# Optimization experiments

Measured on AMD Instinct MI355X. Metric: run time of the kernel, lower is better.

Reference implementation:

```python
import jax, jax.numpy as jnp
import numpy as np

GENE_NUM = 3000
N_NODES = 50000
N_EDGES = 1000000
DIM = 128


def setup_inputs() -> dict:
    key = jax.random.key(0)
    ks = jax.random.split(key, 8)
    h = jax.random.normal(ks[0], (N_NODES, DIM), dtype=jnp.float32)
    alpha = jax.random.normal(ks[1], (GENE_NUM + 2,), dtype=jnp.float32)
    edge_weight = jax.random.uniform(ks[2], (N_EDGES,), dtype=jnp.float32)
    # Xavier-uniform Linear weight, zero bias
    gain = float(np.sqrt(2.0))  # calculate_gain('relu')
    bound = gain * np.sqrt(6.0 / (DIM + DIM))
    W = jax.random.uniform(ks[3], (DIM, DIM), minval=-bound, maxval=bound, dtype=jnp.float32)
    b = jnp.zeros((DIM,), dtype=jnp.float32)
    # node ids: genes 0..GENE_NUM-1 have id = gene index (>=0); cells have id = -1 (<0)
    node_id = jnp.concatenate([
        jnp.arange(GENE_NUM, dtype=jnp.int64),
        -jnp.ones((N_NODES - GENE_NUM,), dtype=jnp.int64),
    ])
    edge_src = jax.random.randint(ks[4], (N_EDGES,), 0, N_NODES, dtype=jnp.int64)
    edge_dst = jax.random.randint(ks[5], (N_EDGES,), 0, N_NODES, dtype=jnp.int64)
    return {"h": h, "alpha": alpha, "edge_weight": edge_weight, "W": W, "b": b,
            "node_id": node_id, "edge_src": edge_src, "edge_dst": edge_dst}


def reference(h, alpha, edge_weight, W, b, node_id, edge_src, edge_dst):
    gene_num = alpha.shape[0] - 2
    src_id = node_id[edge_src]  # [E]
    dst_id = node_id[edge_dst]  # [E]
    # default: cell self-loop alpha -> index gene_num + 1
    idx = jnp.full(edge_src.shape, gene_num + 1, dtype=jnp.int32)
    idx = jnp.where((src_id >= 0) & (dst_id < 0), src_id.astype(jnp.int32), idx)   # gene->cell: beta[src]
    idx = jnp.where((dst_id >= 0) & (src_id < 0), dst_id.astype(jnp.int32), idx)   # cell->gene: beta[dst]
    idx = jnp.where((dst_id >= 0) & (src_id >= 0), gene_num, idx)                  # gene self-loop alpha
    # gather -> per-edge message [E, D]
    coeff = alpha[idx] * edge_weight                     # [E]
    msg = h[edge_src] * coeff[:, None]                   # [E, D]
    # scatter-mean over destination nodes
    n = h.shape[0]
    summ = jax.ops.segment_sum(msg, edge_dst, num_segments=n)           # [N, D]
    cnt = jax.ops.segment_sum(jnp.ones_like(edge_weight), edge_dst, num_segments=n)
    neigh = summ / jnp.maximum(cnt, 1.0)[:, None]
    # MLP: dropout(eval, identity) -> Linear -> ReLU -> norm(identity)
    z = jax.nn.relu(neigh @ W.T + b)
    return z
```

## Files before the change

kernel.cpp:

```cpp
#include <hip/hip_runtime.h>

#define D 128
#define PSHIFT 6
#define PSIZE 64
#define EDGES_PER_BLK 4096
#define CAP 2048
#define MAXPART 1024
#define NCHUNK 4

typedef __attribute__((ext_vector_type(8))) short bf16x8;
typedef __attribute__((ext_vector_type(4))) float f32x4;

__device__ __forceinline__ unsigned short f2bf(float f) {
  unsigned int u = __float_as_uint(f);
  u = (u + 0x7fffu + ((u >> 16) & 1)) >> 16;
  return (unsigned short)u;
}

__global__ __launch_bounds__(512) void cvt_hist_kernel(
    const float* __restrict__ h, unsigned short* __restrict__ h16, int total4,
    const int* __restrict__ edst, int* __restrict__ g_hist, int E,
    int cvtBlocks, int N) {
  if ((int)blockIdx.x < cvtBlocks) {
    int i = blockIdx.x * 512 + threadIdx.x;
    if (i >= total4) return;
    float4 v = ((const float4*)h)[i];
    ushort4 o;
    o.x = f2bf(v.x); o.y = f2bf(v.y); o.z = f2bf(v.z); o.w = f2bf(v.w);
    int f = i * 4;
    int n = f >> 7;
    int d = f & 127;
    int c = d >> 5;
    int wi = d & 31;
    ((ushort4*)h16)[(size_t)c * N * 8 + n * 8 + (wi >> 2)] = o;
    return;
  }
  __shared__ int cnt[MAXPART];
  int t = threadIdx.x;
  cnt[t] = 0; cnt[t + 512] = 0;
  __syncthreads();
  int eb = (blockIdx.x - cvtBlocks) * EDGES_PER_BLK;
#pragma unroll
  for (int q = 0; q < 8; ++q) {
    int e = eb + q * 512 + t;
    if (e < E) atomicAdd(&cnt[edst[e] >> PSHIFT], 1);
  }
  __syncthreads();
  int c = cnt[t];
  if (c > 0) atomicAdd(&g_hist[t], c);
  c = cnt[t + 512];
  if (c > 0) atomicAdd(&g_hist[t + 512], c);
}

__global__ __launch_bounds__(512) void part_scan_kernel(
    const int* __restrict__ g_hist, int* __restrict__ part_off,
    int* __restrict__ g_cursor, int E, int npart) {
  __shared__ int ts[512];
  int t = threadIdx.x;
  int i0 = 2 * t, i1 = 2 * t + 1;
  int v0 = (i0 < npart) ? g_hist[i0] : 0;
  int v1 = (i1 < npart) ? g_hist[i1] : 0;
  ts[t] = v0 + v1;
  __syncthreads();
  for (int off = 1; off < 512; off <<= 1) {
    int x = (t >= off) ? ts[t - off] : 0;
    __syncthreads();
    ts[t] += x;
    __syncthreads();
  }
  int excl = ts[t] - (v0 + v1);
  if (i0 < npart) { part_off[i0] = excl; g_cursor[i0] = excl; }
  if (i1 < npart) { part_off[i1] = excl + v0; g_cursor[i1] = excl + v0; }
  if (t == 0) part_off[npart] = E;
}

__global__ __launch_bounds__(512) void bin_scatter_kernel(
    const float* __restrict__ alpha, const float* __restrict__ ew,
    const int* __restrict__ node_id, const int* __restrict__ esrc,
    const int* __restrict__ edst, int* __restrict__ g_cursor,
    int2* __restrict__ recs, int E, int gene_num) {
  __shared__ int2 lrec[EDGES_PER_BLK];
  __shared__ unsigned short lbin[EDGES_PER_BLK];
  __shared__ int cnt[MAXPART], offl[MAXPART], gbase[MAXPART];
  __shared__ int ts[512];

  int t = threadIdx.x;
  cnt[t] = 0; cnt[t + 512] = 0;
  __syncthreads();

  int eb = blockIdx.x * EDGES_PER_BLK;
  int rx[8]; float rc[8]; int rb[8]; int rk[8];
#pragma unroll
  for (int q = 0; q < 8; ++q) {
    int e = eb + q * 512 + t;
    rk[q] = -1;
    if (e < E) {
      int src = esrc[e];
      int dst = edst[e];
      int sid = node_id[src];
      int did = node_id[dst];
      int idx;
      if (sid >= 0) idx = (did >= 0) ? gene_num : sid;
      else          idx = (did >= 0) ? did : (gene_num + 1);
      rc[q] = alpha[idx] * ew[e];
      rx[q] = src | ((dst & (PSIZE - 1)) << 16);
      int b = dst >> PSHIFT;
      rb[q] = b;
      rk[q] = atomicAdd(&cnt[b], 1);
    }
  }
  __syncthreads();

  int c0 = cnt[2 * t], c1 = cnt[2 * t + 1];
  ts[t] = c0 + c1;
  __syncthreads();
  for (int off = 1; off < 512; off <<= 1) {
    int x = (t >= off) ? ts[t - off] : 0;
    __syncthreads();
    ts[t] += x;
    __syncthreads();
  }
  int exclp = ts[t] - (c0 + c1);
  offl[2 * t] = exclp;
  offl[2 * t + 1] = exclp + c0;
  __syncthreads();

#pragma unroll
  for (int q = 0; q < 8; ++q) {
    if (rk[q] >= 0) {
      int ls = offl[rb[q]] + rk[q];
      lrec[ls] = make_int2(rx[q], __float_as_int(rc[q]));
      lbin[ls] = (unsigned short)rb[q];
    }
  }
  __syncthreads();

  {
    int c = cnt[t];
    if (c > 0) gbase[t] = atomicAdd(&g_cursor[t], c);
    c = cnt[t + 512];
    if (c > 0) gbase[t + 512] = atomicAdd(&g_cursor[t + 512], c);
  }
  __syncthreads();

  int tot = E - eb;
  if (tot > EDGES_PER_BLK) tot = EDGES_PER_BLK;
  for (int s = t; s < tot; s += 512) {
    int b = lbin[s];
    recs[gbase[b] + (s - offl[b])] = lrec[s];
  }
}

__global__ __launch_bounds__(512) void part_acc_kernel(
    const unsigned short* __restrict__ h16, const int2* __restrict__ recs,
    const int* __restrict__ part_off, float* __restrict__ neigh, int N) {
  __shared__ int2 lrec[CAP];
  __shared__ int cnt[PSIZE], offl[PSIZE];

  int t = threadIdx.x;
  int p = blockIdx.x >> 2;
  int chunk = blockIdx.x & 3;
  if (t < PSIZE) cnt[t] = 0;
  __syncthreads();

  int start = part_off[p];
  int R = part_off[p + 1] - start;
  if (R > CAP) R = CAP;

  int2 rq[4]; int dlq[4]; int rkq[4];
#pragma unroll
  for (int q = 0; q < 4; ++q) {
    int s = q * 512 + t;
    rkq[q] = -1;
    if (s < R) {
      int2 r = recs[start + s];
      rq[q] = r;
      int dl = (r.x >> 16) & (PSIZE - 1);
      dlq[q] = dl;
      rkq[q] = atomicAdd(&cnt[dl], 1);
    }
  }
  __syncthreads();

  if (t < PSIZE) offl[t] = cnt[t];
  __syncthreads();
  for (int off = 1; off < PSIZE; off <<= 1) {
    int x = 0;
    if (t < PSIZE && t >= off) x = offl[t - off];
    __syncthreads();
    if (t < PSIZE) offl[t] += x;
    __syncthreads();
  }
  if (t < PSIZE) offl[t] -= cnt[t];
  __syncthreads();

#pragma unroll
  for (int q = 0; q < 4; ++q)
    if (rkq[q] >= 0) lrec[offl[dlq[q]] + rkq[q]] = rq[q];
  __syncthreads();

  int w = t >> 6;
  int l = t & 63;
  int esub = l >> 4;
  int dpair = l & 15;
  const unsigned int* hp = ((const unsigned int*)h16) + (size_t)chunk * N * 16 + dpair;

  for (int dd = 0; dd < 4; ++dd) {
    int dlA = w * 8 + 2 * dd;
    int dlB = dlA + 1;
    int cA = cnt[dlA], oA = offl[dlA];
    int cB = cnt[dlB], oB = offl[dlB];
    float axA = 0.f, ayA = 0.f, axB = 0.f, ayB = 0.f;
    int cmax = (cA > cB) ? cA : cB;
    for (int k = 0; k < cmax; k += 16) {
      float cfA[4], cfB[4];
      unsigned int vA[4], vB[4];
      int aA[4], aB[4];
#pragma unroll
      for (int q = 0; q < 4; ++q) {
        int sl = k + 4 * q + esub;
        int iA = oA + sl; iA = (iA < CAP) ? iA : (CAP - 1);
        int iB = oB + sl; iB = (iB < CAP) ? iB : (CAP - 1);
        int2 rA = lrec[iA];
        int2 rB = lrec[iB];
        bool okA = sl < cA;
        bool okB = sl < cB;
        aA[q] = okA ? (rA.x & 0xffff) : 0;
        aB[q] = okB ? (rB.x & 0xffff) : 0;
        cfA[q] = okA ? __int_as_float(rA.y) : 0.f;
        cfB[q] = okB ? __int_as_float(rB.y) : 0.f;
      }
#pragma unroll
      for (int q = 0; q < 4; ++q) {
        vA[q] = hp[(size_t)aA[q] * 16];
        vB[q] = hp[(size_t)aB[q] * 16];
      }
#pragma unroll
      for (int q = 0; q < 4; ++q) {
        axA += cfA[q] * __uint_as_float(vA[q] << 16);
        ayA += cfA[q] * __uint_as_float(vA[q] & 0xffff0000u);
        axB += cfB[q] * __uint_as_float(vB[q] << 16);
        ayB += cfB[q] * __uint_as_float(vB[q] & 0xffff0000u);
      }
    }
    axA += __shfl_xor(axA, 16); ayA += __shfl_xor(ayA, 16);
    axB += __shfl_xor(axB, 16); ayB += __shfl_xor(ayB, 16);
    axA += __shfl_xor(axA, 32); ayA += __shfl_xor(ayA, 32);
    axB += __shfl_xor(axB, 32); ayB += __shfl_xor(ayB, 32);

    int dstA = p * PSIZE + dlA;
    int dstB = p * PSIZE + dlB;
    if (l < 16) {
      if (dstA < N) {
        float inv = 1.0f / (float)(cA > 0 ? cA : 1);
        ((float2*)neigh)[(size_t)dstA * 64 + chunk * 16 + dpair] =
            make_float2(axA * inv, ayA * inv);
      }
      if (dstB < N) {
        float inv = 1.0f / (float)(cB > 0 ? cB : 1);
        ((float2*)neigh)[(size_t)dstB * 64 + chunk * 16 + dpair] =
            make_float2(axB * inv, ayB * inv);
      }
    }
  }
}

__global__ __launch_bounds__(256) void mlp_mfma_kernel(
    const float* __restrict__ W, const float* __restrict__ bias,
    float* __restrict__ io, int N) {
  __shared__ __align__(16) unsigned short Wl[128 * 128];

  int t = threadIdx.x;
#pragma unroll
  for (int i = 0; i < 8; ++i) {
    int chunk = t + 256 * i;
    int row = chunk >> 4;
    int cb = chunk & 15;
    const float* gp = W + (size_t)row * 128 + cb * 8;
    float4 a = *(const float4*)gp;
    float4 b = *(const float4*)(gp + 4);
    bf16x8 v;
    v[0] = (short)f2bf(a.x); v[1] = (short)f2bf(a.y);
    v[2] = (short)f2bf(a.z); v[3] = (short)f2bf(a.w);
    v[4] = (short)f2bf(b.x); v[5] = (short)f2bf(b.y);
    v[6] = (short)f2bf(b.z); v[7] = (short)f2bf(b.w);
    *(bf16x8*)((char*)Wl + row * 256 + ((cb ^ (row & 7)) << 4)) = v;
  }
  __syncthreads();

  int l = t & 63;
  int w = t >> 6;
  int kg = l >> 4;
  int m_base = blockIdx.x * 64 + w * 16;
  int arow = m_base + (l & 15);
  if (arow >= N) arow = N - 1;

  bf16x8 af[4];
  const float* ap = io + (size_t)arow * 128 + kg * 8;
#pragma unroll
  for (int kk = 0; kk < 4; ++kk) {
    float4 a = *(const float4*)(ap + kk * 32);
    float4 b = *(const float4*)(ap + kk * 32 + 4);
    bf16x8 v;
    v[0] = (short)f2bf(a.x); v[1] = (short)f2bf(a.y);
    v[2] = (short)f2bf(a.z); v[3] = (short)f2bf(a.w);
    v[4] = (short)f2bf(b.x); v[5] = (short)f2bf(b.y);
    v[6] = (short)f2bf(b.z); v[7] = (short)f2bf(b.w);
    af[kk] = v;
  }

#pragma unroll
  for (int c = 0; c < 8; ++c) {
    f32x4 acc = {0.f, 0.f, 0.f, 0.f};
    int row_w = c * 16 + (l & 15);
    int rs = row_w & 7;
#pragma unroll
    for (int kk = 0; kk < 4; ++kk) {
      int cb = kk * 4 + kg;
      bf16x8 bf = *(bf16x8*)((char*)Wl + row_w * 256 + ((cb ^ rs) << 4));
      acc = __builtin_amdgcn_mfma_f32_16x16x32_bf16(af[kk], bf, acc, 0, 0, 0);
    }
    int j = c * 16 + (l & 15);
    float bj = bias[j];
#pragma unroll
    for (int r = 0; r < 4; ++r) {
      int m = m_base + kg * 4 + r;
      if (m < N) io[(size_t)m * 128 + j] = fmaxf(acc[r] + bj, 0.0f);
    }
  }
}

extern "C" void kernel_launch(void* const* d_in, const int* in_sizes, int n_in,
                              void* d_out, int out_size, void* d_ws, size_t ws_size,
                              hipStream_t stream) {
  const float* h     = (const float*)d_in[0];
  const float* alpha = (const float*)d_in[1];
  const float* ew    = (const float*)d_in[2];
  const float* W     = (const float*)d_in[3];
  const float* bias  = (const float*)d_in[4];
  const int* node_id = (const int*)d_in[5];
  const int* esrc    = (const int*)d_in[6];
  const int* edst    = (const int*)d_in[7];
  float* out = (float*)d_out;

  int E = in_sizes[2];
  int N = in_sizes[5];
  int gene_num = in_sizes[1] - 2;
  int npart = (N + PSIZE - 1) / PSIZE;
  int eblocks = (E + EDGES_PER_BLK - 1) / EDGES_PER_BLK;
  int total4 = N * D / 4;
  int cvtBlocks = (total4 + 511) / 512;

  int* g_hist   = (int*)d_ws;
  int* part_off = g_hist + MAXPART;
  int* g_cursor = part_off + MAXPART + 1;
  size_t h16_off = ((size_t)(3 * MAXPART + 1) * sizeof(int) + 15) & ~(size_t)15;
  unsigned short* h16 = (unsigned short*)((char*)d_ws + h16_off);
  size_t rec_off = (h16_off + (size_t)N * D * sizeof(unsigned short) + 15) & ~(size_t)15;
  int2* recs = (int2*)((char*)d_ws + rec_off);
  size_t need = rec_off + (size_t)E * sizeof(int2);
  if (ws_size < need) return;

  hipMemsetAsync(g_hist, 0, MAXPART * sizeof(int), stream);

  cvt_hist_kernel<<<cvtBlocks + eblocks, 512, 0, stream>>>(
      h, h16, total4, edst, g_hist, E, cvtBlocks, N);
  part_scan_kernel<<<1, 512, 0, stream>>>(g_hist, part_off, g_cursor, E, npart);
  bin_scatter_kernel<<<eblocks, 512, 0, stream>>>(alpha, ew, node_id, esrc,
                                                  edst, g_cursor, recs, E,
                                                  gene_num);
  part_acc_kernel<<<npart * NCHUNK, 512, 0, stream>>>(h16, recs, part_off, out, N);
  {
    int blocks = (N + 63) / 64;
    mlp_mfma_kernel<<<blocks, 256, 0, stream>>>(W, bias, out, N);
  }
}
```

Measured before the change: 117.8 us.

## Split per-partition local sort into its own kernel and pad segments to 16

The per-destination local sort that each of the four chunk blocks repeated is moved into a separate sort_kernel run once per partition. It writes the sorted records back and stores per-node counts and offsets to the workspace. The accumulation kernel now loads the pre-sorted records into zero-padded 16-aligned segments, which removes the per-element bounds clamps and lets each of the two destinations skip its loads once its own segment is done. This costs an extra kernel launch, an extra global read and write of the record array, and more shared memory per block.

```diff
diff --git a/kernel.cpp b/kernel.cpp
--- a/kernel.cpp
+++ b/kernel.cpp
@@ -5,6 +5,7 @@
 #define PSIZE 64
 #define EDGES_PER_BLK 4096
 #define CAP 2048
+#define CAPP 3072
 #define MAXPART 1024
 #define NCHUNK 4
 
@@ -151,15 +152,14 @@
   }
 }
 
-__global__ __launch_bounds__(512) void part_acc_kernel(
-    const unsigned short* __restrict__ h16, const int2* __restrict__ recs,
-    const int* __restrict__ part_off, float* __restrict__ neigh, int N) {
+__global__ __launch_bounds__(512) void sort_kernel(
+    int2* __restrict__ recs, const int* __restrict__ part_off,
+    int* __restrict__ cnt_g, int* __restrict__ off_g) {
   __shared__ int2 lrec[CAP];
   __shared__ int cnt[PSIZE], offl[PSIZE];
 
   int t = threadIdx.x;
-  int p = blockIdx.x >> 2;
-  int chunk = blockIdx.x & 3;
+  int p = blockIdx.x;
   if (t < PSIZE) cnt[t] = 0;
   __syncthreads();
 
@@ -199,48 +199,109 @@
     if (rkq[q] >= 0) lrec[offl[dlq[q]] + rkq[q]] = rq[q];
   __syncthreads();
 
+  for (int s = t; s < R; s += 512) recs[start + s] = lrec[s];
+  if (t < PSIZE) {
+    cnt_g[p * PSIZE + t] = cnt[t];
+    off_g[p * PSIZE + t] = offl[t];
+  }
+}
+
+__global__ __launch_bounds__(512) void part_acc_kernel(
+    const unsigned short* __restrict__ h16, const int2* __restrict__ recs,
+    const int* __restrict__ part_off, const int* __restrict__ cnt_g,
+    const int* __restrict__ off_g, float* __restrict__ neigh, int N) {
+  __shared__ int2 lrec[CAPP];
+  __shared__ int cnt[PSIZE], offl[PSIZE], padoff[PSIZE];
+
+  int t = threadIdx.x;
+  int p = blockIdx.x >> 2;
+  int chunk = blockIdx.x & 3;
+
+  int start = part_off[p];
+  int R = part_off[p + 1] - start;
+  if (R > CAP) R = CAP;
+
+  if (t < PSIZE) {
+    cnt[t] = cnt_g[p * PSIZE + t];
+    offl[t] = off_g[p * PSIZE + t];
+    padoff[t] = (cnt[t] + 15) & ~15;
+  }
+  {
+    int2 z = make_int2(0, 0);
+#pragma unroll
+    for (int q = 0; q < CAPP / 512; ++q) lrec[q * 512 + t] = z;
+  }
+  __syncthreads();
+  for (int off = 1; off < PSIZE; off <<= 1) {
+    int x = 0;
+    if (t < PSIZE && t >= off) x = padoff[t - off];
+    __syncthreads();
+    if (t < PSIZE) padoff[t] += x;
+    __syncthreads();
+  }
+  if (t < PSIZE) padoff[t] -= (cnt[t] + 15) & ~15;
+  __syncthreads();
+
+  for (int s = t; s < R; s += 512) {
+    int2 r = recs[start + s];
+    int dl = (r.x >> 16) & (PSIZE - 1);
+    lrec[padoff[dl] + (s - offl[dl])] = r;
+  }
+  __syncthreads();
+
   int w = t >> 6;
   int l = t & 63;
   int esub = l >> 4;
   int dpair = l & 15;
-  const unsigned int* hp = ((const unsigned int*)h16) + (size_t)chunk * N * 16 + dpair;
+  const unsigned int* hp =
+      ((const unsigned int*)h16) + (size_t)chunk * N * 16 + dpair;
 
   for (int dd = 0; dd < 4; ++dd) {
     int dlA = w * 8 + 2 * dd;
     int dlB = dlA + 1;
-    int cA = cnt[dlA], oA = offl[dlA];
-    int cB = cnt[dlB], oB = offl[dlB];
+    int cA = cnt[dlA], cB = cnt[dlB];
+    int oA = padoff[dlA], oB = padoff[dlB];
+    int cpA = (cA + 15) & ~15, cpB = (cB + 15) & ~15;
     float axA = 0.f, ayA = 0.f, axB = 0.f, ayB = 0.f;
-    int cmax = (cA > cB) ? cA : cB;
-    for (int k = 0; k < cmax; k += 16) {
+    int cpm = (cpA > cpB) ? cpA : cpB;
+    for (int k = 0; k < cpm; k += 16) {
+      bool doA = k < cpA;
+      bool doB = k < cpB;
+      unsigned int aA[4], aB[4], vA[4], vB[4];
       float cfA[4], cfB[4];
-      unsigned int vA[4], vB[4];
-      int aA[4], aB[4];
-#pragma unroll
-      for (int q = 0; q < 4; ++q) {
-        int sl = k + 4 * q + esub;
-        int iA = oA + sl; iA = (iA < CAP) ? iA : (CAP - 1);
-        int iB = oB + sl; iB = (iB < CAP) ? iB : (CAP - 1);
-        int2 rA = lrec[iA];
-        int2 rB = lrec[iB];
-        bool okA = sl < cA;
-        bool okB = sl < cB;
-        aA[q] = okA ? (rA.x & 0xffff) : 0;
-        aB[q] = okB ? (rB.x & 0xffff) : 0;
-        cfA[q] = okA ? __int_as_float(rA.y) : 0.f;
-        cfB[q] = okB ? __int_as_float(rB.y) : 0.f;
-      }
-#pragma unroll
-      for (int q = 0; q < 4; ++q) {
-        vA[q] = hp[(size_t)aA[q] * 16];
-        vB[q] = hp[(size_t)aB[q] * 16];
-      }
-#pragma unroll
-      for (int q = 0; q < 4; ++q) {
-        axA += cfA[q] * __uint_as_float(vA[q] << 16);
-        ayA += cfA[q] * __uint_as_float(vA[q] & 0xffff0000u);
-        axB += cfB[q] * __uint_as_float(vB[q] << 16);
-        ayB += cfB[q] * __uint_as_float(vB[q] & 0xffff0000u);
+      if (doA) {
+#pragma unroll
+        for (int q = 0; q < 4; ++q) {
+          int2 r = lrec[oA + k + 4 * q + esub];
+          aA[q] = r.x & 0xffff;
+          cfA[q] = __int_as_float(r.y);
+        }
+#pragma unroll
+        for (int q = 0; q < 4; ++q) vA[q] = hp[(size_t)aA[q] * 16];
+      }
+      if (doB) {
+#pragma unroll
+        for (int q = 0; q < 4; ++q) {
+          int2 r = lrec[oB + k + 4 * q + esub];
+          aB[q] = r.x & 0xffff;
+          cfB[q] = __int_as_float(r.y);
+        }
+#pragma unroll
+        for (int q = 0; q < 4; ++q) vB[q] = hp[(size_t)aB[q] * 16];
+      }
+      if (doA) {
+#pragma unroll
+        for (int q = 0; q < 4; ++q) {
+          axA += cfA[q] * __uint_as_float(vA[q] << 16);
+          ayA += cfA[q] * __uint_as_float(vA[q] & 0xffff0000u);
+        }
+      }
+      if (doB) {
+#pragma unroll
+        for (int q = 0; q < 4; ++q) {
+          axB += cfB[q] * __uint_as_float(vB[q] << 16);
+          ayB += cfB[q] * __uint_as_float(vB[q] & 0xffff0000u);
+        }
       }
     }
     axA += __shfl_xor(axA, 16); ayA += __shfl_xor(ayA, 16);
@@ -354,7 +415,10 @@
   int* g_hist   = (int*)d_ws;
   int* part_off = g_hist + MAXPART;
   int* g_cursor = part_off + MAXPART + 1;
-  size_t h16_off = ((size_t)(3 * MAXPART + 1) * sizeof(int) + 15) & ~(size_t)15;
+  int* cnt_g    = g_cursor + MAXPART;
+  int* off_g    = cnt_g + MAXPART * PSIZE;
+  size_t h16_off = ((size_t)(3 * MAXPART + 1 + 2 * MAXPART * PSIZE) * sizeof(int)
+                    + 15) & ~(size_t)15;
   unsigned short* h16 = (unsigned short*)((char*)d_ws + h16_off);
   size_t rec_off = (h16_off + (size_t)N * D * sizeof(unsigned short) + 15) & ~(size_t)15;
   int2* recs = (int2*)((char*)d_ws + rec_off);
@@ -369,7 +433,9 @@
   bin_scatter_kernel<<<eblocks, 512, 0, stream>>>(alpha, ew, node_id, esrc,
                                                   edst, g_cursor, recs, E,
                                                   gene_num);
-  part_acc_kernel<<<npart * NCHUNK, 512, 0, stream>>>(h16, recs, part_off, out, N);
+  sort_kernel<<<npart, 512, 0, stream>>>(recs, part_off, cnt_g, off_g);
+  part_acc_kernel<<<npart * NCHUNK, 512, 0, stream>>>(h16, recs, part_off,
+                                                      cnt_g, off_g, out, N);
   {
     int blocks = (N + 63) / 64;
     mlp_mfma_kernel<<<blocks, 256, 0, stream>>>(W, bias, out, N);
```

Measured after the change: 116.7 us. About the same (-0.9%).

## Sort records once per partition in separate kernel and pad per-destination lists

Applied to the files above, without the earlier changes.

Moves the per-partition counting sort of edge records by destination out of the accumulation kernel into a new sort_kernel. It runs once per partition instead of once per feature chunk, and writes the sorted records plus count, offset and padded-offset tables back to global memory. The accumulation kernel then places records into a zero-initialised shared buffer with each destination's list padded to a multiple of four. One 16-lane group then walks one destination's list without per-element bounds checks. This removes the four-fold redundant sort and the masking overhead, at the cost of an extra launch, an extra global round trip for the records, and possible load imbalance between destinations of different degree.

```diff
diff --git a/kernel.cpp b/kernel.cpp
--- a/kernel.cpp
+++ b/kernel.cpp
@@ -5,6 +5,7 @@
 #define PSIZE 64
 #define EDGES_PER_BLK 4096
 #define CAP 2048
+#define CAPP 2244
 #define MAXPART 1024
 #define NCHUNK 4
 
@@ -151,15 +152,15 @@
   }
 }
 
-__global__ __launch_bounds__(512) void part_acc_kernel(
-    const unsigned short* __restrict__ h16, const int2* __restrict__ recs,
-    const int* __restrict__ part_off, float* __restrict__ neigh, int N) {
+__global__ __launch_bounds__(512) void sort_kernel(
+    int2* __restrict__ recs, const int* __restrict__ part_off,
+    int* __restrict__ cnt_g, int* __restrict__ off_g,
+    int* __restrict__ pad_g) {
   __shared__ int2 lrec[CAP];
-  __shared__ int cnt[PSIZE], offl[PSIZE];
-
-  int t = threadIdx.x;
-  int p = blockIdx.x >> 2;
-  int chunk = blockIdx.x & 3;
+  __shared__ int cnt[PSIZE], offl[PSIZE], padl[PSIZE];
+
+  int t = threadIdx.x;
+  int p = blockIdx.x;
   if (t < PSIZE) cnt[t] = 0;
   __syncthreads();
 
@@ -182,85 +183,107 @@
   }
   __syncthreads();
 
-  if (t < PSIZE) offl[t] = cnt[t];
+  if (t < PSIZE) { offl[t] = cnt[t]; padl[t] = (cnt[t] + 3) & ~3; }
   __syncthreads();
   for (int off = 1; off < PSIZE; off <<= 1) {
-    int x = 0;
-    if (t < PSIZE && t >= off) x = offl[t - off];
-    __syncthreads();
-    if (t < PSIZE) offl[t] += x;
-    __syncthreads();
-  }
-  if (t < PSIZE) offl[t] -= cnt[t];
+    int x = 0, y = 0;
+    if (t < PSIZE && t >= off) { x = offl[t - off]; y = padl[t - off]; }
+    __syncthreads();
+    if (t < PSIZE) { offl[t] += x; padl[t] += y; }
+    __syncthreads();
+  }
+  if (t < PSIZE) {
+    offl[t] -= cnt[t];
+    padl[t] -= (cnt[t] + 3) & ~3;
+  }
   __syncthreads();
 
 #pragma unroll
   for (int q = 0; q < 4; ++q)
     if (rkq[q] >= 0) lrec[offl[dlq[q]] + rkq[q]] = rq[q];
+  __syncthreads();
+
+  for (int s = t; s < R; s += 512) recs[start + s] = lrec[s];
+  if (t < PSIZE) {
+    cnt_g[p * PSIZE + t] = cnt[t];
+    off_g[p * PSIZE + t] = offl[t];
+    pad_g[p * PSIZE + t] = padl[t];
+  }
+}
+
+__global__ __launch_bounds__(512) void part_acc_kernel(
+    const unsigned short* __restrict__ h16, const int2* __restrict__ recs,
+    const int* __restrict__ part_off, const int* __restrict__ cnt_g,
+    const int* __restrict__ off_g, const int* __restrict__ pad_g,
+    float* __restrict__ neigh, int N) {
+  __shared__ int2 lrec[CAPP];
+  __shared__ int cnt[PSIZE], offl[PSIZE], padl[PSIZE];
+
+  int t = threadIdx.x;
+  int p = blockIdx.x >> 2;
+  int chunk = blockIdx.x & 3;
+
+  int start = part_off[p];
+  int R = part_off[p + 1] - start;
+  if (R > CAP) R = CAP;
+
+  if (t < PSIZE) {
+    cnt[t] = cnt_g[p * PSIZE + t];
+    offl[t] = off_g[p * PSIZE + t];
+    padl[t] = pad_g[p * PSIZE + t];
+  }
+  {
+    int2 z = make_int2(0, 0);
+    for (int q = t; q < CAPP; q += 512) lrec[q] = z;
+  }
+  __syncthreads();
+
+  for (int s = t; s < R; s += 512) {
+    int2 r = recs[start + s];
+    int dl = (r.x >> 16) & (PSIZE - 1);
+    lrec[padl[dl] + (s - offl[dl])] = r;
+  }
   __syncthreads();
 
   int w = t >> 6;
   int l = t & 63;
   int esub = l >> 4;
   int dpair = l & 15;
-  const unsigned int* hp = ((const unsigned int*)h16) + (size_t)chunk * N * 16 + dpair;
-
-  for (int dd = 0; dd < 4; ++dd) {
-    int dlA = w * 8 + 2 * dd;
-    int dlB = dlA + 1;
-    int cA = cnt[dlA], oA = offl[dlA];
-    int cB = cnt[dlB], oB = offl[dlB];
-    float axA = 0.f, ayA = 0.f, axB = 0.f, ayB = 0.f;
-    int cmax = (cA > cB) ? cA : cB;
-    for (int k = 0; k < cmax; k += 16) {
-      float cfA[4], cfB[4];
-      unsigned int vA[4], vB[4];
-      int aA[4], aB[4];
-#pragma unroll
-      for (int q = 0; q < 4; ++q) {
-        int sl = k + 4 * q + esub;
-        int iA = oA + sl; iA = (iA < CAP) ? iA : (CAP - 1);
-        int iB = oB + sl; iB = (iB < CAP) ? iB : (CAP - 1);
-        int2 rA = lrec[iA];
-        int2 rB = lrec[iB];
-        bool okA = sl < cA;
-        bool okB = sl < cB;
-        aA[q] = okA ? (rA.x & 0xffff) : 0;
-        aB[q] = okB ? (rB.x & 0xffff) : 0;
-        cfA[q] = okA ? __int_as_float(rA.y) : 0.f;
-        cfB[q] = okB ? __int_as_float(rB.y) : 0.f;
-      }
-#pragma unroll
-      for (int q = 0; q < 4; ++q) {
-        vA[q] = hp[(size_t)aA[q] * 16];
-        vB[q] = hp[(size_t)aB[q] * 16];
-      }
-#pragma unroll
-      for (int q = 0; q < 4; ++q) {
-        axA += cfA[q] * __uint_as_float(vA[q] << 16);
-        ayA += cfA[q] * __uint_as_float(vA[q] & 0xffff0000u);
-        axB += cfB[q] * __uint_as_float(vB[q] << 16);
-        ayB += cfB[q] * __uint_as_float(vB[q] & 0xffff0000u);
-      }
-    }
-    axA += __shfl_xor(axA, 16); ayA += __shfl_xor(ayA, 16);
-    axB += __shfl_xor(axB, 16); ayB += __shfl_xor(ayB, 16);
-    axA += __shfl_xor(axA, 32); ayA += __shfl_xor(ayA, 32);
-    axB += __shfl_xor(axB, 32); ayB += __shfl_xor(ayB, 32);
-
-    int dstA = p * PSIZE + dlA;
-    int dstB = p * PSIZE + dlB;
-    if (l < 16) {
-      if (dstA < N) {
-        float inv = 1.0f / (float)(cA > 0 ? cA : 1);
-        ((float2*)neigh)[(size_t)dstA * 64 + chunk * 16 + dpair] =
-            make_float2(axA * inv, ayA * inv);
-      }
-      if (dstB < N) {
-        float inv = 1.0f / (float)(cB > 0 ? cB : 1);
-        ((float2*)neigh)[(size_t)dstB * 64 + chunk * 16 + dpair] =
-            make_float2(axB * inv, ayB * inv);
-      }
+  const unsigned int* hpc =
+      ((const unsigned int*)h16) + (size_t)chunk * N * 16 + dpair;
+
+#pragma unroll
+  for (int h2 = 0; h2 < 2; ++h2) {
+    int myDl = w * 8 + h2 * 4 + esub;
+    int myCnt = cnt[myDl];
+    int myOff = padl[myDl];
+    int myPad = (myCnt + 3) & ~3;
+    float ax = 0.f, ay = 0.f;
+    for (int k = 0; k < myPad; k += 4) {
+      int2 r0 = lrec[myOff + k + 0];
+      int2 r1 = lrec[myOff + k + 1];
+      int2 r2 = lrec[myOff + k + 2];
+      int2 r3 = lrec[myOff + k + 3];
+      unsigned int v0 = hpc[(size_t)(r0.x & 0xffff) * 16];
+      unsigned int v1 = hpc[(size_t)(r1.x & 0xffff) * 16];
+      unsigned int v2 = hpc[(size_t)(r2.x & 0xffff) * 16];
+      unsigned int v3 = hpc[(size_t)(r3.x & 0xffff) * 16];
+      float c0 = __int_as_float(r0.y), c1 = __int_as_float(r1.y);
+      float c2 = __int_as_float(r2.y), c3 = __int_as_float(r3.y);
+      ax += c0 * __uint_as_float(v0 << 16);
+      ay += c0 * __uint_as_float(v0 & 0xffff0000u);
+      ax += c1 * __uint_as_float(v1 << 16);
+      ay += c1 * __uint_as_float(v1 & 0xffff0000u);
+      ax += c2 * __uint_as_float(v2 << 16);
+      ay += c2 * __uint_as_float(v2 & 0xffff0000u);
+      ax += c3 * __uint_as_float(v3 << 16);
+      ay += c3 * __uint_as_float(v3 & 0xffff0000u);
+    }
+    int dst = p * PSIZE + myDl;
+    if (dst < N) {
+      float inv = 1.0f / (float)(myCnt > 0 ? myCnt : 1);
+      ((float2*)neigh)[(size_t)dst * 64 + chunk * 16 + dpair] =
+          make_float2(ax * inv, ay * inv);
     }
   }
 }
@@ -354,7 +377,11 @@
   int* g_hist   = (int*)d_ws;
   int* part_off = g_hist + MAXPART;
   int* g_cursor = part_off + MAXPART + 1;
-  size_t h16_off = ((size_t)(3 * MAXPART + 1) * sizeof(int) + 15) & ~(size_t)15;
+  int* cnt_g    = g_cursor + MAXPART;
+  int* off_g    = cnt_g + MAXPART * PSIZE;
+  int* pad_g    = off_g + MAXPART * PSIZE;
+  size_t h16_off = ((size_t)(3 * MAXPART + 1 + 3 * MAXPART * PSIZE) * sizeof(int)
+                    + 15) & ~(size_t)15;
   unsigned short* h16 = (unsigned short*)((char*)d_ws + h16_off);
   size_t rec_off = (h16_off + (size_t)N * D * sizeof(unsigned short) + 15) & ~(size_t)15;
   int2* recs = (int2*)((char*)d_ws + rec_off);
@@ -369,7 +396,10 @@
   bin_scatter_kernel<<<eblocks, 512, 0, stream>>>(alpha, ew, node_id, esrc,
                                                   edst, g_cursor, recs, E,
                                                   gene_num);
-  part_acc_kernel<<<npart * NCHUNK, 512, 0, stream>>>(h16, recs, part_off, out, N);
+  sort_kernel<<<npart, 512, 0, stream>>>(recs, part_off, cnt_g, off_g, pad_g);
+  part_acc_kernel<<<npart * NCHUNK, 512, 0, stream>>>(h16, recs, part_off,
+                                                      cnt_g, off_g, pad_g,
+                                                      out, N);
   {
     int blocks = (N + 63) / 64;
     mlp_mfma_kernel<<<blocks, 256, 0, stream>>>(W, bias, out, N);
```

Measured after the change: 108.3 us. 1.09x faster.
